# Kernel optimization log

Hardware: AMD Instinct MI355X
Metric: run time of the kernel (lower is better)

Reference implementation:

```python
import jax, jax.numpy as jnp
import numpy as np

V, B, L, NG = 50000, 128, 350, 3        # vocab, batch(docs), doc length, n-gram window
D, H, C = 768, 256, 20                  # bert dim, num_hidden, class_num
HEADS, LAYERS, K, ALPHA = 8, 2, 3, 0.15 # GAT heads/layers, diffusion hops k, alpha


def setup_inputs() -> dict:
    rng = np.random.default_rng(0)
    # per-doc graphs: 350 unique word-ids per doc (nodes), n-gram window edges
    node_ids = np.stack([rng.choice(V, L, replace=False) for _ in range(B)]).ravel()
    src_b, dst_b = [], []
    for i in range(L):
        for j in range(max(0, i - NG), min(L, i + NG + 1)):
            src_b.append(i); dst_b.append(j)
    src_b, dst_b = np.asarray(src_b), np.asarray(dst_b)
    off = (np.arange(B) * L)[:, None]
    edge_src = (src_b[None, :] + off).ravel()
    edge_dst = (dst_b[None, :] + off).ravel()
    graph_id = np.repeat(np.arange(B), L)

    ks = jax.random.split(jax.random.key(0), 8)
    f32 = jnp.float32
    return {
        'node_ids': jnp.asarray(node_ids, jnp.int32),
        'edge_src': jnp.asarray(edge_src, jnp.int32),
        'edge_dst': jnp.asarray(edge_dst, jnp.int32),
        'graph_id': jnp.asarray(graph_id, jnp.int32),
        'emb':    (jax.random.normal(ks[0], (V, D), f32) * 0.02),
        'W1':     (jax.random.normal(ks[1], (D, H), f32) / np.sqrt(D)).astype(f32),
        'b1':     jnp.zeros((H,), f32),
        'W2':     (jax.random.normal(ks[2], (H, C), f32) / np.sqrt(H)).astype(f32),
        'b2':     jnp.zeros((C,), f32),
        'gat_W':  (jax.random.normal(ks[3], (LAYERS, HEADS, C, C), f32) / np.sqrt(C)).astype(f32),
        'a_src':  (jax.random.normal(ks[4], (LAYERS, HEADS, C), f32) * 0.1),
        'a_dst':  (jax.random.normal(ks[5], (LAYERS, HEADS, C), f32) * 0.1),
        'w_gate': (jax.random.normal(ks[6], (C,), f32) / np.sqrt(C)).astype(f32),
        'b_gate': jnp.zeros((), f32),
    }


def _gat_layer(h, W, a_s, a_d, src, dst, N):
    # h: [N,C]; W: [Hd,C,C]; a_s/a_d: [Hd,C]
    z = jnp.einsum('nc,hcd->hnd', h, W)                     # [Hd,N,C]
    e = jax.nn.leaky_relu(jnp.einsum('hnd,hd->hn', z, a_s)[:, src]
                          + jnp.einsum('hnd,hd->hn', z, a_d)[:, dst], 0.2)  # [Hd,E]

    def segsoftmax(ev):  # edge softmax over incoming edges at each dst node
        m = jax.ops.segment_max(ev, dst, num_segments=N)
        ex = jnp.exp(ev - m[dst])
        s = jax.ops.segment_sum(ex, dst, num_segments=N)
        return ex / (s[dst] + 1e-9)

    att = jax.vmap(segsoftmax)(e)                           # [Hd,E]

    def diffuse(zh, ah):  # attention diffusion: Z_t = (1-a) A Z_{t-1} + a Z_0
        zt = zh
        for _ in range(K):
            agg = jax.ops.segment_sum(ah[:, None] * zt[src], dst, num_segments=N)
            zt = (1.0 - ALPHA) * agg + ALPHA * zh
        return zt

    out = jax.vmap(diffuse)(z, att)                         # [Hd,N,C]
    return jax.nn.elu(out).mean(axis=0)                     # merge='mean'


def reference(node_ids, edge_src, edge_dst, graph_id, emb, W1, b1, W2, b2,
              gat_W, a_src, a_dst, w_gate, b_gate):
    N = node_ids.shape[0]
    x = emb[node_ids]                                       # [N,768] gather
    x = jax.nn.relu(x @ W1 + b1)                            # linear1 + ReLU
    h = x @ W2 + b2                                         # linear2 -> [N,C]
    for l in range(LAYERS):
        h = _gat_layer(h, gat_W[l], a_src[l], a_dst[l], edge_src, edge_dst, N)
    gate = jax.nn.sigmoid(h @ w_gate + b_gate)[:, None]     # WeightAndSum gate
    return jax.ops.segment_sum(gate * h, graph_id, num_segments=B)  # [B,C]
```

## Files before the change

kernel.cpp:

```cpp
#include <hip/hip_runtime.h>
#include <hip/hip_bf16.h>
#include <cstddef>

#define NB_NODES 44800
#define NDOCS 128
#define DLEN 350
#define DIM 768
#define HID 256
#define NCLS 20
#define NHEADS 8
#define ZSTR 24

typedef __bf16 v8bf __attribute__((ext_vector_type(8)));
typedef __bf16 v4bf __attribute__((ext_vector_type(4)));
typedef float v4f __attribute__((ext_vector_type(4)));

__global__ __launch_bounds__(256) void k_transpose(const float* __restrict__ W1,
                                                   __bf16* __restrict__ W1T) {
  int idx = blockIdx.x * 256 + threadIdx.x;
  int n = idx / 768, k = idx - n * 768;
  W1T[idx] = (__bf16)W1[k * 256 + n];
}

__global__ __launch_bounds__(256) void k_mlp(
    const int* __restrict__ node_ids, const float* __restrict__ emb,
    const __bf16* __restrict__ W1T, const float* __restrict__ b1,
    const float* __restrict__ W2, const float* __restrict__ b2,
    float* __restrict__ h0) {
  __shared__ __align__(16) char smem[43520];
  __bf16* As = (__bf16*)smem;
  float*  xs = (float*)smem;
  __bf16* w2s = (__bf16*)(smem + 33280);
  int tid = threadIdx.x;
  int wave = tid >> 6, lane = tid & 63;
  int quad = lane >> 4, l16 = lane & 15;
  int m0 = blockIdx.x * 64;

  int lrow = tid & 15;
  int lk4  = (tid >> 4) & 3;
  int khalf = (tid >> 6) & 1;
  int msubA = tid >> 7;
  int kbase = khalf * 32 + lk4 * 8;
  const float* apA = emb + (size_t)node_ids[m0 + msubA * 16 + lrow] * DIM + kbase;
  const float* apB = emb + (size_t)node_ids[m0 + (msubA + 2) * 16 + lrow] * DIM + kbase;

  v4f acc[4][4];
#pragma unroll
  for (int ms = 0; ms < 4; ++ms)
#pragma unroll
    for (int j = 0; j < 4; ++j) acc[ms][j] = (v4f){0.f, 0.f, 0.f, 0.f};

  v4f pf[4];
  pf[0] = *(const v4f*)(apA); pf[1] = *(const v4f*)(apA + 4);
  pf[2] = *(const v4f*)(apB); pf[3] = *(const v4f*)(apB + 4);

  for (int kc = 0; kc < 12; ++kc) {
    __bf16* buf = As + (kc & 1) * 4096;
    v8bf w0, w1;
#pragma unroll
    for (int e = 0; e < 4; ++e) {
      w0[e] = (__bf16)pf[0][e]; w0[4 + e] = (__bf16)pf[1][e];
      w1[e] = (__bf16)pf[2][e]; w1[4 + e] = (__bf16)pf[3][e];
    }
    *(v8bf*)(buf + tid * 8) = w0;
    *(v8bf*)(buf + tid * 8 + 2048) = w1;
    if (kc < 11) {
      int k1 = (kc + 1) * 64;
      pf[0] = *(const v4f*)(apA + k1); pf[1] = *(const v4f*)(apA + k1 + 4);
      pf[2] = *(const v4f*)(apB + k1); pf[3] = *(const v4f*)(apB + k1 + 4);
    }
    __syncthreads();

#pragma unroll
    for (int ks = 0; ks < 2; ++ks) {
      v8bf af[4], bv[4];
#pragma unroll
      for (int ms = 0; ms < 4; ++ms)
        af[ms] = *(const v8bf*)(buf + ((ms * 2 + ks) * 64 + lane) * 8);
#pragma unroll
      for (int j = 0; j < 4; ++j)
        bv[j] = *(const v8bf*)(W1T + (size_t)(wave * 64 + j * 16 + l16) * DIM + kc * 64 + ks * 32 + quad * 8);
#pragma unroll
      for (int ms = 0; ms < 4; ++ms)
#pragma unroll
        for (int j = 0; j < 4; ++j)
          acc[ms][j] = __builtin_amdgcn_mfma_f32_16x16x32_bf16(af[ms], bv[j], acc[ms][j], 0, 0, 0);
    }
  }

  __syncthreads();
  for (int i = tid; i < HID * NCLS; i += 256) w2s[i] = (__bf16)W2[i];

#pragma unroll
  for (int p = 0; p < 2; ++p) {
    if (p) __syncthreads();
#pragma unroll
    for (int mh = 0; mh < 2; ++mh) {
      int ms = p * 2 + mh;
#pragma unroll
      for (int j = 0; j < 4; ++j) {
        int col = wave * 64 + j * 16 + l16;
        float bb = b1[col];
#pragma unroll
        for (int r = 0; r < 4; ++r) {
          int lr = mh * 16 + quad * 4 + r;
          float v = acc[ms][j][r] + bb;
          xs[lr * 260 + col] = v > 0.f ? v : 0.f;
        }
      }
    }
    __syncthreads();
    if (tid < 160) {
      int m = tid / 5, c0 = (tid % 5) * 4;
      v4f s = *(const v4f*)(b2 + c0);
      for (int k = 0; k < HID; ++k) {
        float x = xs[m * 260 + k];
        v4bf w = *(const v4bf*)(w2s + k * NCLS + c0);
        s[0] += x * (float)w[0]; s[1] += x * (float)w[1];
        s[2] += x * (float)w[2]; s[3] += x * (float)w[3];
      }
      *(v4f*)(h0 + (size_t)(m0 + p * 32 + m) * NCLS + c0) = s;
    }
  }
}

__global__ __launch_bounds__(384) void k_gat(
    const float* __restrict__ hin, const float* __restrict__ gatW,
    const float* __restrict__ a_src, const float* __restrict__ a_dst,
    int layer, float* __restrict__ zout) {
  __shared__ float zA[DLEN * ZSTR];
  __shared__ float asv[DLEN], adv[DLEN];
  int tid = threadIdx.x;
  int head = blockIdx.x & 7;
  int doc = blockIdx.x >> 3;
  const float* W  = gatW  + (size_t)(layer * NHEADS + head) * NCLS * NCLS;
  const float* av = a_src + (layer * NHEADS + head) * NCLS;
  const float* dv = a_dst + (layer * NHEADS + head) * NCLS;
  int r = tid;
  bool act = r < DLEN;

  float z0[NCLS];
  if (act) {
    const float* hr = hin + ((size_t)doc * DLEN + r) * NCLS;
    float h[NCLS];
#pragma unroll
    for (int q = 0; q < 5; ++q) {
      v4f t = *(const v4f*)(hr + q * 4);
#pragma unroll
      for (int e = 0; e < 4; ++e) h[q * 4 + e] = t[e];
    }
    float zacc[NCLS];
#pragma unroll
    for (int d = 0; d < NCLS; ++d) zacc[d] = 0.f;
#pragma unroll
    for (int c = 0; c < NCLS; ++c) {
      float hc = h[c];
#pragma unroll
      for (int d = 0; d < NCLS; ++d) zacc[d] += hc * W[c * NCLS + d];
    }
    float sa = 0.f, sd = 0.f;
#pragma unroll
    for (int d = 0; d < NCLS; ++d) { sa += zacc[d] * av[d]; sd += zacc[d] * dv[d]; }
    asv[r] = sa; adv[r] = sd;
#pragma unroll
    for (int q = 0; q < 5; ++q) {
      v4f t;
#pragma unroll
      for (int e = 0; e < 4; ++e) t[e] = zacc[q * 4 + e];
      *(v4f*)(zA + r * ZSTR + q * 4) = t;
    }
#pragma unroll
    for (int d = 0; d < NCLS; ++d) z0[d] = zacc[d];
  }
  __syncthreads();

  float att[7];
  if (act) {
    float ad = adv[r];
    float e[7]; float m = -1e30f;
#pragma unroll
    for (int j = 0; j < 7; ++j) {
      int s = r - 3 + j;
      bool valid = (s >= 0) && (s < DLEN);
      float x = valid ? asv[s] + ad : -1e30f;
      x = x > 0.f ? x : 0.2f * x;
      e[j] = valid ? x : -1e30f;
      if (e[j] > m) m = e[j];
    }
    float sum = 0.f;
#pragma unroll
    for (int j = 0; j < 7; ++j) {
      float ex = (e[j] > -1e29f) ? expf(e[j] - m) : 0.f;
      e[j] = ex; sum += ex;
    }
    float inv = 1.f / (sum + 1e-9f);
#pragma unroll
    for (int j = 0; j < 7; ++j) att[j] = e[j] * inv;
  }

  float vn[NCLS];
  for (int hop = 0; hop < 3; ++hop) {
    if (act) {
      v4f agg[5];
#pragma unroll
      for (int q = 0; q < 5; ++q) agg[q] = (v4f){0.f, 0.f, 0.f, 0.f};
#pragma unroll
      for (int j = 0; j < 7; ++j) {
        int s = r - 3 + j;
        s = s < 0 ? 0 : (s > DLEN - 1 ? DLEN - 1 : s);
        float a = att[j];
#pragma unroll
        for (int q = 0; q < 5; ++q) {
          v4f zq = *(const v4f*)(zA + s * ZSTR + q * 4);
#pragma unroll
          for (int e = 0; e < 4; ++e) agg[q][e] += a * zq[e];
        }
      }
#pragma unroll
      for (int q = 0; q < 5; ++q)
#pragma unroll
        for (int e = 0; e < 4; ++e)
          vn[q * 4 + e] = 0.85f * agg[q][e] + 0.15f * z0[q * 4 + e];
    }
    if (hop < 2) {
      __syncthreads();
      if (act) {
#pragma unroll
        for (int q = 0; q < 5; ++q) {
          v4f t;
#pragma unroll
          for (int e = 0; e < 4; ++e) t[e] = vn[q * 4 + e];
          *(v4f*)(zA + r * ZSTR + q * 4) = t;
        }
      }
      __syncthreads();
    }
  }

  if (act) {
    float* og = zout + ((size_t)head * NB_NODES + (size_t)doc * DLEN + r) * NCLS;
#pragma unroll
    for (int q = 0; q < 5; ++q) {
      v4f t;
#pragma unroll
      for (int e = 0; e < 4; ++e) {
        float x = vn[q * 4 + e];
        t[e] = x > 0.f ? x : expf(x) - 1.f;
      }
      *(v4f*)(og + q * 4) = t;
    }
  }
}

__global__ __launch_bounds__(256) void k_headmean(
    const float* __restrict__ eluzt, float* __restrict__ hout) {
  int idx = blockIdx.x * 256 + threadIdx.x;
  v4f s = (v4f){0.f, 0.f, 0.f, 0.f};
#pragma unroll
  for (int h = 0; h < NHEADS; ++h)
    s += ((const v4f*)eluzt)[(size_t)h * (NB_NODES * NCLS / 4) + idx];
  v4f o; o[0] = s[0] * 0.125f; o[1] = s[1] * 0.125f; o[2] = s[2] * 0.125f; o[3] = s[3] * 0.125f;
  ((v4f*)hout)[idx] = o;
}

__global__ __launch_bounds__(64) void k_pool(
    const float* __restrict__ hfin, const float* __restrict__ w_gate,
    const float* __restrict__ b_gate, float* __restrict__ out) {
  int b = blockIdx.x, lane = threadIdx.x;
  float wg[NCLS];
#pragma unroll
  for (int c = 0; c < NCLS; ++c) wg[c] = w_gate[c];
  float bg = b_gate[0];
  float acc[NCLS];
#pragma unroll
  for (int c = 0; c < NCLS; ++c) acc[c] = 0.f;
  for (int n = lane; n < DLEN; n += 64) {
    const v4f* hr = (const v4f*)(hfin + ((size_t)b * DLEN + n) * NCLS);
    float hv[NCLS];
    float d = bg;
#pragma unroll
    for (int q = 0; q < 5; ++q) {
      v4f t = hr[q];
#pragma unroll
      for (int j = 0; j < 4; ++j) { hv[q * 4 + j] = t[j]; d += t[j] * wg[q * 4 + j]; }
    }
    float g = 1.f / (1.f + expf(-d));
#pragma unroll
    for (int c = 0; c < NCLS; ++c) acc[c] += g * hv[c];
  }
#pragma unroll
  for (int off = 32; off > 0; off >>= 1)
#pragma unroll
    for (int c = 0; c < NCLS; ++c) acc[c] += __shfl_down(acc[c], off);
  if (lane == 0)
#pragma unroll
    for (int c = 0; c < NCLS; ++c) out[b * NCLS + c] = acc[c];
}

extern "C" void kernel_launch(void* const* d_in, const int* in_sizes, int n_in,
                              void* d_out, int out_size, void* d_ws, size_t ws_size,
                              hipStream_t stream) {
  const int* node_ids = (const int*)d_in[0];
  const float* emb    = (const float*)d_in[4];
  const float* W1     = (const float*)d_in[5];
  const float* b1     = (const float*)d_in[6];
  const float* W2     = (const float*)d_in[7];
  const float* b2     = (const float*)d_in[8];
  const float* gatW   = (const float*)d_in[9];
  const float* a_src  = (const float*)d_in[10];
  const float* a_dst  = (const float*)d_in[11];
  const float* w_gate = (const float*)d_in[12];
  const float* b_gate = (const float*)d_in[13];
  float* out = (float*)d_out;
  char* ws = (char*)d_ws;

  __bf16* W1T = (__bf16*)(ws + 0);
  float* hA  = (float*)(ws + 393216);
  float* hB  = (float*)(ws + 3977216);
  float* zt  = (float*)(ws + 7561216);

  k_transpose<<<768, 256, 0, stream>>>(W1, W1T);
  k_mlp<<<NB_NODES / 64, 256, 0, stream>>>(node_ids, emb, W1T, b1, W2, b2, hA);
  k_gat<<<NDOCS * NHEADS, 384, 0, stream>>>(hA, gatW, a_src, a_dst, 0, zt);
  k_headmean<<<(NB_NODES * NCLS / 4) / 256, 256, 0, stream>>>(zt, hB);
  k_gat<<<NDOCS * NHEADS, 384, 0, stream>>>(hB, gatW, a_src, a_dst, 1, zt);
  k_headmean<<<(NB_NODES * NCLS / 4) / 256, 256, 0, stream>>>(zt, hA);
  k_pool<<<NDOCS, 64, 0, stream>>>(hA, w_gate, b_gate, out);
}
```

Baseline: 361.3 us.

## Shrink MLP shared memory, transpose GAT LDS layout, fuse final headmean into pooling

The MLP epilogue now processes 16-row slices instead of 32, which shrinks shared memory so the kernel can declare 5 blocks per CU in its launch bounds. The GAT kernel stores z in a channel-major LDS layout so neighbouring threads read consecutive addresses, replacing strided vector loads. The last head-mean kernel is fused into the pooling kernel, which drops one launch and one global round trip for the head-averaged features. The trade-offs are more barriers in the MLP epilogue and scalar LDS accesses in GAT.

```diff
diff --git a/kernel.cpp b/kernel.cpp
--- a/kernel.cpp
+++ b/kernel.cpp
@@ -9,11 +9,13 @@
 #define HID 256
 #define NCLS 20
 #define NHEADS 8
-#define ZSTR 24
+#define ZROW 352
 
 typedef __bf16 v8bf __attribute__((ext_vector_type(8)));
 typedef __bf16 v4bf __attribute__((ext_vector_type(4)));
+typedef __bf16 v2bf __attribute__((ext_vector_type(2)));
 typedef float v4f __attribute__((ext_vector_type(4)));
+typedef float v2f __attribute__((ext_vector_type(2)));
 
 __global__ __launch_bounds__(256) void k_transpose(const float* __restrict__ W1,
                                                    __bf16* __restrict__ W1T) {
@@ -22,15 +24,15 @@
   W1T[idx] = (__bf16)W1[k * 256 + n];
 }
 
-__global__ __launch_bounds__(256) void k_mlp(
+__global__ __launch_bounds__(256, 5) void k_mlp(
     const int* __restrict__ node_ids, const float* __restrict__ emb,
     const __bf16* __restrict__ W1T, const float* __restrict__ b1,
     const float* __restrict__ W2, const float* __restrict__ b2,
     float* __restrict__ h0) {
-  __shared__ __align__(16) char smem[43520];
+  __shared__ __align__(16) char smem[26880];
   __bf16* As = (__bf16*)smem;
   float*  xs = (float*)smem;
-  __bf16* w2s = (__bf16*)(smem + 33280);
+  __bf16* w2s = (__bf16*)(smem + 16640);
   int tid = threadIdx.x;
   int wave = tid >> 6, lane = tid & 63;
   int quad = lane >> 4, l16 = lane & 15;
@@ -92,34 +94,30 @@
   for (int i = tid; i < HID * NCLS; i += 256) w2s[i] = (__bf16)W2[i];
 
 #pragma unroll
-  for (int p = 0; p < 2; ++p) {
-    if (p) __syncthreads();
-#pragma unroll
-    for (int mh = 0; mh < 2; ++mh) {
-      int ms = p * 2 + mh;
-#pragma unroll
-      for (int j = 0; j < 4; ++j) {
-        int col = wave * 64 + j * 16 + l16;
-        float bb = b1[col];
-#pragma unroll
-        for (int r = 0; r < 4; ++r) {
-          int lr = mh * 16 + quad * 4 + r;
-          float v = acc[ms][j][r] + bb;
-          xs[lr * 260 + col] = v > 0.f ? v : 0.f;
-        }
+  for (int ms = 0; ms < 4; ++ms) {
+    __syncthreads();
+#pragma unroll
+    for (int j = 0; j < 4; ++j) {
+      int col = wave * 64 + j * 16 + l16;
+      float bb = b1[col];
+#pragma unroll
+      for (int r = 0; r < 4; ++r) {
+        int lr = quad * 4 + r;
+        float v = acc[ms][j][r] + bb;
+        xs[lr * 260 + col] = v > 0.f ? v : 0.f;
       }
     }
     __syncthreads();
     if (tid < 160) {
-      int m = tid / 5, c0 = (tid % 5) * 4;
-      v4f s = *(const v4f*)(b2 + c0);
+      int m = tid / 10, c0 = (tid % 10) * 2;
+      float s0 = b2[c0], s1 = b2[c0 + 1];
       for (int k = 0; k < HID; ++k) {
         float x = xs[m * 260 + k];
-        v4bf w = *(const v4bf*)(w2s + k * NCLS + c0);
-        s[0] += x * (float)w[0]; s[1] += x * (float)w[1];
-        s[2] += x * (float)w[2]; s[3] += x * (float)w[3];
-      }
-      *(v4f*)(h0 + (size_t)(m0 + p * 32 + m) * NCLS + c0) = s;
+        v2bf w = *(const v2bf*)(w2s + k * NCLS + c0);
+        s0 += x * (float)w[0]; s1 += x * (float)w[1];
+      }
+      v2f o; o[0] = s0; o[1] = s1;
+      *(v2f*)(h0 + (size_t)(m0 + ms * 16 + m) * NCLS + c0) = o;
     }
   }
 }
@@ -128,7 +126,7 @@
     const float* __restrict__ hin, const float* __restrict__ gatW,
     const float* __restrict__ a_src, const float* __restrict__ a_dst,
     int layer, float* __restrict__ zout) {
-  __shared__ float zA[DLEN * ZSTR];
+  __shared__ float zT[NCLS * ZROW];
   __shared__ float asv[DLEN], adv[DLEN];
   int tid = threadIdx.x;
   int head = blockIdx.x & 7;
@@ -163,12 +161,7 @@
     for (int d = 0; d < NCLS; ++d) { sa += zacc[d] * av[d]; sd += zacc[d] * dv[d]; }
     asv[r] = sa; adv[r] = sd;
 #pragma unroll
-    for (int q = 0; q < 5; ++q) {
-      v4f t;
-#pragma unroll
-      for (int e = 0; e < 4; ++e) t[e] = zacc[q * 4 + e];
-      *(v4f*)(zA + r * ZSTR + q * 4) = t;
-    }
+    for (int c = 0; c < NCLS; ++c) zT[c * ZROW + r] = zacc[c];
 #pragma unroll
     for (int d = 0; d < NCLS; ++d) z0[d] = zacc[d];
   }
@@ -201,37 +194,25 @@
   float vn[NCLS];
   for (int hop = 0; hop < 3; ++hop) {
     if (act) {
-      v4f agg[5];
-#pragma unroll
-      for (int q = 0; q < 5; ++q) agg[q] = (v4f){0.f, 0.f, 0.f, 0.f};
+      float agg[NCLS];
+#pragma unroll
+      for (int c = 0; c < NCLS; ++c) agg[c] = 0.f;
 #pragma unroll
       for (int j = 0; j < 7; ++j) {
         int s = r - 3 + j;
         s = s < 0 ? 0 : (s > DLEN - 1 ? DLEN - 1 : s);
         float a = att[j];
 #pragma unroll
-        for (int q = 0; q < 5; ++q) {
-          v4f zq = *(const v4f*)(zA + s * ZSTR + q * 4);
-#pragma unroll
-          for (int e = 0; e < 4; ++e) agg[q][e] += a * zq[e];
-        }
-      }
-#pragma unroll
-      for (int q = 0; q < 5; ++q)
-#pragma unroll
-        for (int e = 0; e < 4; ++e)
-          vn[q * 4 + e] = 0.85f * agg[q][e] + 0.15f * z0[q * 4 + e];
+        for (int c = 0; c < NCLS; ++c) agg[c] += a * zT[c * ZROW + s];
+      }
+#pragma unroll
+      for (int c = 0; c < NCLS; ++c) vn[c] = 0.85f * agg[c] + 0.15f * z0[c];
     }
     if (hop < 2) {
       __syncthreads();
       if (act) {
 #pragma unroll
-        for (int q = 0; q < 5; ++q) {
-          v4f t;
-#pragma unroll
-          for (int e = 0; e < 4; ++e) t[e] = vn[q * 4 + e];
-          *(v4f*)(zA + r * ZSTR + q * 4) = t;
-        }
+        for (int c = 0; c < NCLS; ++c) zT[c * ZROW + r] = vn[c];
       }
       __syncthreads();
     }
@@ -263,38 +244,57 @@
   ((v4f*)hout)[idx] = o;
 }
 
-__global__ __launch_bounds__(64) void k_pool(
-    const float* __restrict__ hfin, const float* __restrict__ w_gate,
+__global__ __launch_bounds__(384) void k_hm_pool(
+    const float* __restrict__ eluzt, const float* __restrict__ w_gate,
     const float* __restrict__ b_gate, float* __restrict__ out) {
-  int b = blockIdx.x, lane = threadIdx.x;
+  __shared__ float red[6][NCLS];
+  int tid = threadIdx.x;
+  int doc = blockIdx.x;
+  int r = tid;
+  bool act = r < DLEN;
+
   float wg[NCLS];
 #pragma unroll
   for (int c = 0; c < NCLS; ++c) wg[c] = w_gate[c];
-  float bg = b_gate[0];
-  float acc[NCLS];
-#pragma unroll
-  for (int c = 0; c < NCLS; ++c) acc[c] = 0.f;
-  for (int n = lane; n < DLEN; n += 64) {
-    const v4f* hr = (const v4f*)(hfin + ((size_t)b * DLEN + n) * NCLS);
-    float hv[NCLS];
-    float d = bg;
-#pragma unroll
-    for (int q = 0; q < 5; ++q) {
-      v4f t = hr[q];
-#pragma unroll
-      for (int j = 0; j < 4; ++j) { hv[q * 4 + j] = t[j]; d += t[j] * wg[q * 4 + j]; }
-    }
+  float contrib[NCLS];
+#pragma unroll
+  for (int c = 0; c < NCLS; ++c) contrib[c] = 0.f;
+  if (act) {
+    float hm[NCLS];
+#pragma unroll
+    for (int c = 0; c < NCLS; ++c) hm[c] = 0.f;
+#pragma unroll
+    for (int hd = 0; hd < NHEADS; ++hd) {
+      const float* p = eluzt + ((size_t)hd * NB_NODES + (size_t)doc * DLEN + r) * NCLS;
+#pragma unroll
+      for (int q = 0; q < 5; ++q) {
+        v4f t = *(const v4f*)(p + q * 4);
+#pragma unroll
+        for (int e = 0; e < 4; ++e) hm[q * 4 + e] += t[e];
+      }
+    }
+    float d = b_gate[0];
+#pragma unroll
+    for (int c = 0; c < NCLS; ++c) { hm[c] *= 0.125f; d += hm[c] * wg[c]; }
     float g = 1.f / (1.f + expf(-d));
 #pragma unroll
-    for (int c = 0; c < NCLS; ++c) acc[c] += g * hv[c];
+    for (int c = 0; c < NCLS; ++c) contrib[c] = g * hm[c];
   }
 #pragma unroll
   for (int off = 32; off > 0; off >>= 1)
 #pragma unroll
-    for (int c = 0; c < NCLS; ++c) acc[c] += __shfl_down(acc[c], off);
+    for (int c = 0; c < NCLS; ++c) contrib[c] += __shfl_down(contrib[c], off);
+  int wave = tid >> 6, lane = tid & 63;
   if (lane == 0)
 #pragma unroll
-    for (int c = 0; c < NCLS; ++c) out[b * NCLS + c] = acc[c];
+    for (int c = 0; c < NCLS; ++c) red[wave][c] = contrib[c];
+  __syncthreads();
+  if (tid < NCLS) {
+    float s = 0.f;
+#pragma unroll
+    for (int w = 0; w < 6; ++w) s += red[w][tid];
+    out[doc * NCLS + tid] = s;
+  }
 }
 
 extern "C" void kernel_launch(void* const* d_in, const int* in_sizes, int n_in,
@@ -324,6 +324,5 @@
   k_gat<<<NDOCS * NHEADS, 384, 0, stream>>>(hA, gatW, a_src, a_dst, 0, zt);
   k_headmean<<<(NB_NODES * NCLS / 4) / 256, 256, 0, stream>>>(zt, hB);
   k_gat<<<NDOCS * NHEADS, 384, 0, stream>>>(hB, gatW, a_src, a_dst, 1, zt);
-  k_headmean<<<(NB_NODES * NCLS / 4) / 256, 256, 0, stream>>>(zt, hA);
-  k_pool<<<NDOCS, 64, 0, stream>>>(hA, w_gate, b_gate, out);
-}
+  k_hm_pool<<<NDOCS, 384, 0, stream>>>(zt, w_gate, b_gate, out);
+}
```

New measurement: 435.8 us. 1.21x slower.
